# Optimization experiments

Hardware: AMD Instinct MI355X
Metric: run time of the kernel (lower is better)

## Reference

```python
import jax, jax.numpy as jnp
import numpy as np

T = 16000        # signal length
N1 = 120         # first-order filters (J=12, Q=10)
NPSI2 = 14       # second-order filterbank size (Q2=1)
NPAIR = 553      # second-order coefficients -> 120 + 553 = 673 channels
SUB1 = 8         # subsample U1 before order 2
T2 = T // SUB1   # 2000
STR1 = 1000      # lowpass stride at length T  -> 16 output samples
STR2 = T2 // (T // STR1)  # 125 -> 16 output samples
LOG_EPS = 1e-6
BN_EPS = 1e-5


def _gauss_hat(N, xi, sigma):
    om = np.arange(N) / N
    return np.exp(-((om - xi) ** 2) / (2.0 * sigma ** 2)).astype(np.float32)


def _filterbank():
    Q = 10.0
    xi1 = 0.45 * 2.0 ** (-np.arange(N1) / Q)
    sig1 = np.maximum(xi1 * 0.1, 2.0 / T)
    psi1 = np.stack([_gauss_hat(T, x, s) for x, s in zip(xi1, sig1)])
    phi1 = _gauss_hat(T, 0.0, 0.4 / STR1)
    xi2 = 0.45 * 2.0 ** (-np.arange(NPSI2, dtype=np.float64))
    sig2 = np.maximum(xi2 * 0.2, 2.0 / T2)
    psi2 = np.stack([_gauss_hat(T2, x, s) for x, s in zip(xi2, sig2)])
    phi2 = _gauss_hat(T2, 0.0, 0.4 / STR2)
    pairs = [(i, j) for i in range(N1) for j in range(NPSI2) if xi2[j] < xi1[i] / 2.0]
    pairs = pairs[:NPAIR]
    assert len(pairs) == NPAIR
    pi1 = np.array([p[0] for p in pairs], np.int32)
    pi2 = np.array([p[1] for p in pairs], np.int32)
    return psi1, phi1, psi2, phi2, pi1, pi2


def setup_inputs():
    key = jax.random.key(0)
    ks = jax.random.split(key, 8)
    psi1, phi1, psi2, phi2, pi1, pi2 = _filterbank()
    B = 32
    inp = {
        "x": jax.random.normal(ks[0], (B, 1, T), jnp.float32),
        "psi1_hat": jnp.asarray(psi1),
        "phi1_hat": jnp.asarray(phi1),
        "psi2_hat": jnp.asarray(psi2),
        "phi2_hat": jnp.asarray(phi2),
        "gamma": jnp.ones((673,), jnp.float32),
        "beta": jnp.zeros((673,), jnp.float32),
        "W1": jax.random.normal(ks[1], (300, 673), jnp.float32) * 0.04,
        "b1": jnp.zeros((300,), jnp.float32),
        "W2": jax.random.normal(ks[2], (90, 300), jnp.float32) * 0.06,
        "b2": jnp.zeros((90,), jnp.float32),
        "W3": jax.random.normal(ks[3], (35, 90), jnp.float32) * 0.1,
        "b3": jnp.zeros((35,), jnp.float32),
        "pair_i1": jnp.asarray(pi1),
        "pair_i2": jnp.asarray(pi2),
    }
    return inp


def reference(x, psi1_hat, phi1_hat, psi2_hat, phi2_hat, gamma, beta,
              W1, b1, W2, b2, W3, b3, pair_i1, pair_i2):
    xs = x.squeeze(1)                                       # [B, T]
    Xf = jnp.fft.fft(xs)                                    # [B, T] c64
    # --- order 1: wavelet conv (freq-domain), modulus ---
    U1 = jnp.abs(jnp.fft.ifft(Xf[:, None, :] * psi1_hat[None]))        # [B, N1, T]
    # S1 = lowpass(U1) subsampled to 16 samples
    S1 = jnp.real(jnp.fft.ifft(jnp.fft.fft(U1) * phi1_hat))[..., ::STR1]  # [B, N1, 16]
    # --- order 2 on subsampled U1 ---
    U1sf = jnp.fft.fft(U1[..., ::SUB1])                     # [B, N1, T2]
    U2 = jnp.abs(jnp.fft.ifft(U1sf[:, pair_i1, :] * psi2_hat[pair_i2]))  # [B, NPAIR, T2]
    S2 = jnp.real(jnp.fft.ifft(jnp.fft.fft(U2) * phi2_hat))[..., ::STR2]  # [B, NPAIR, 16]
    S = jnp.concatenate([S1, S2], axis=1)                   # [B, 673, 16]
    # log-abs + temporal mean pooling
    f = jnp.mean(jnp.log(jnp.abs(S) + LOG_EPS), axis=-1)    # [B, 673]
    # BatchNorm1d (training mode: batch statistics)
    mu = jnp.mean(f, axis=0)
    var = jnp.var(f, axis=0)
    f = (f - mu) / jnp.sqrt(var + BN_EPS) * gamma + beta
    # MLP head
    h = jax.nn.relu(f @ W1.T + b1)
    h = jax.nn.relu(h @ W2.T + b2)
    return jax.nn.log_softmax(h @ W3.T + b3, axis=-1)
```

## Files before the change

kernel.cpp:

```cpp
#include <hip/hip_runtime.h>
#include <math.h>

typedef float2 cf;

__device__ __forceinline__ cf cadd(cf a, cf b){ return make_float2(a.x+b.x, a.y+b.y); }
__device__ __forceinline__ cf csub(cf a, cf b){ return make_float2(a.x-b.x, a.y-b.y); }
__device__ __forceinline__ cf cmul(cf a, cf b){ return make_float2(a.x*b.x - a.y*b.y, a.x*b.y + a.y*b.x); }

__device__ __forceinline__ int SW(int i){ return i ^ ((i>>4)&15); }
#define AT(x) s[SW(x)]
#define WFENCE asm volatile("" ::: "memory")

template<bool WAVE> __device__ __forceinline__ void SYf(){
  if constexpr (WAVE) { WFENCE; } else __syncthreads();
}

__device__ __forceinline__ int devB(int i){
  int jm = i/10 + 2;
  double kc = 900.0*exp2((double)(-jm));
  double sg = fmax(180.0*exp2((double)(-jm)), 2.0);
  return min(2000, (int)ceil(kc + 6.5*sg) + 1);
}

template<int N, int L, bool INV>
__device__ __forceinline__ void stage_r2(cf* __restrict__ s, const cf* __restrict__ tw, int tid, int nt){
  constexpr int Ls = L/2, nbf = N/2, tws = 16000/L;
  for (int q = tid; q < nbf; q += nt){
    int blk = q / Ls, j = q - blk*Ls;
    int base = blk*L + j;
    cf w1 = tw[tws*j]; if (INV) w1.y = -w1.y;
    if (!INV){
      cf a = AT(base), b = AT(base+Ls);
      AT(base) = cadd(a,b);
      AT(base+Ls) = cmul(csub(a,b), w1);
    } else {
      cf a = AT(base), b = cmul(AT(base+Ls), w1);
      AT(base) = cadd(a,b);
      AT(base+Ls) = csub(a,b);
    }
  }
}

template<int N, int L, bool INV>
__device__ __forceinline__ void stage_r4(cf* __restrict__ s, const cf* __restrict__ tw, int tid, int nt){
  constexpr int Ls = L/4, nbf = N/4, tws = 16000/L;
  for (int q = tid; q < nbf; q += nt){
    int blk = q / Ls, j = q - blk*Ls;
    int base = blk*L + j;
    cf w1 = tw[tws*j]; if (INV) w1.y = -w1.y;
    cf w2 = cmul(w1,w1), w3 = cmul(w2,w1);
    if (!INV){
      cf y0=AT(base), y1=AT(base+Ls), y2=AT(base+2*Ls), y3=AT(base+3*Ls);
      cf t0=cadd(y0,y2), t1=csub(y0,y2), t2=cadd(y1,y3), t3=csub(y1,y3);
      AT(base)      = cadd(t0,t2);
      AT(base+Ls)   = cmul(make_float2(t1.x + t3.y, t1.y - t3.x), w1);
      AT(base+2*Ls) = cmul(csub(t0,t2), w2);
      AT(base+3*Ls) = cmul(make_float2(t1.x - t3.y, t1.y + t3.x), w3);
    } else {
      cf z0=AT(base);
      cf z1=cmul(AT(base+Ls),   w1);
      cf z2=cmul(AT(base+2*Ls), w2);
      cf z3=cmul(AT(base+3*Ls), w3);
      cf t0=cadd(z0,z2), t1=csub(z0,z2), t2=cadd(z1,z3), t3=csub(z1,z3);
      AT(base)      = cadd(t0,t2);
      AT(base+Ls)   = make_float2(t1.x - t3.y, t1.y + t3.x);
      AT(base+2*Ls) = csub(t0,t2);
      AT(base+3*Ls) = make_float2(t1.x + t3.y, t1.y - t3.x);
    }
  }
}

template<int N, int L, bool INV>
__device__ __forceinline__ void stage_r5(cf* __restrict__ s, const cf* __restrict__ tw, int tid, int nt){
  constexpr int Ls = L/5, nbf = N/5, tws = 16000/L;
  const float C1 = 0.30901699437494742f, S1c = 0.95105651629515357f;
  const float C2 = -0.80901699437494745f, S2c = 0.58778525229247314f;
  for (int q = tid; q < nbf; q += nt){
    int blk = q / Ls, j = q - blk*Ls;
    int base = blk*L + j;
    cf w1 = tw[tws*j]; if (INV) w1.y = -w1.y;
    cf w2 = cmul(w1,w1), w3 = cmul(w2,w1), w4 = cmul(w2,w2);
    if (!INV){
      cf y0=AT(base), y1=AT(base+Ls), y2=AT(base+2*Ls), y3=AT(base+3*Ls), y4=AT(base+4*Ls);
      cf t1=cadd(y1,y4), t2=csub(y1,y4), t3=cadd(y2,y3), t4=csub(y2,y3);
      cf z0 = cadd(y0, cadd(t1,t3));
      cf m1 = make_float2(y0.x + C1*t1.x + C2*t3.x, y0.y + C1*t1.y + C2*t3.y);
      cf m2 = make_float2(y0.x + C2*t1.x + C1*t3.x, y0.y + C2*t1.y + C1*t3.y);
      cf wa = make_float2(S1c*t2.x + S2c*t4.x, S1c*t2.y + S2c*t4.y);
      cf wb = make_float2(S2c*t2.x - S1c*t4.x, S2c*t2.y - S1c*t4.y);
      cf o1 = make_float2(m1.x + wa.y, m1.y - wa.x);
      cf o4 = make_float2(m1.x - wa.y, m1.y + wa.x);
      cf o2 = make_float2(m2.x + wb.y, m2.y - wb.x);
      cf o3 = make_float2(m2.x - wb.y, m2.y + wb.x);
      AT(base) = z0;
      AT(base+Ls)   = cmul(o1,w1);
      AT(base+2*Ls) = cmul(o2,w2);
      AT(base+3*Ls) = cmul(o3,w3);
      AT(base+4*Ls) = cmul(o4,w4);
    } else {
      cf z0=AT(base);
      cf z1=cmul(AT(base+Ls),   w1);
      cf z2=cmul(AT(base+2*Ls), w2);
      cf z3=cmul(AT(base+3*Ls), w3);
      cf z4=cmul(AT(base+4*Ls), w4);
      cf t1=cadd(z1,z4), t2=csub(z1,z4), t3=cadd(z2,z3), t4=csub(z2,z3);
      cf y0 = cadd(z0, cadd(t1,t3));
      cf m1 = make_float2(z0.x + C1*t1.x + C2*t3.x, z0.y + C1*t1.y + C2*t3.y);
      cf m2 = make_float2(z0.x + C2*t1.x + C1*t3.x, z0.y + C2*t1.y + C1*t3.y);
      cf wa = make_float2(S1c*t2.x + S2c*t4.x, S1c*t2.y + S2c*t4.y);
      cf wb = make_float2(S2c*t2.x - S1c*t4.x, S2c*t2.y - S1c*t4.y);
      AT(base)      = y0;
      AT(base+Ls)   = make_float2(m1.x - wa.y, m1.y + wa.x);
      AT(base+2*Ls) = make_float2(m2.x - wb.y, m2.y + wb.x);
      AT(base+3*Ls) = make_float2(m2.x + wb.y, m2.y - wb.x);
      AT(base+4*Ls) = make_float2(m1.x + wa.y, m1.y - wa.x);
    }
  }
}

template<int N, int L, bool INV>
__device__ __forceinline__ void stage_r8(cf* __restrict__ s, const cf* __restrict__ tw, int tid, int nt){
  constexpr int Ls = L/8, nbf = N/8, tws = 16000/L;
  const float RC = 0.70710678118654752f;
  for (int q = tid; q < nbf; q += nt){
    int blk = q / Ls, j = q - blk*Ls;
    int base = blk*L + j;
    cf w1 = tw[tws*j]; if (INV) w1.y = -w1.y;
    cf w2 = cmul(w1,w1), w3 = cmul(w2,w1), w4 = cmul(w2,w2);
    cf w5 = cmul(w4,w1), w6 = cmul(w3,w3), w7 = cmul(w4,w3);
    if (!INV){
      cf y0=AT(base), y1=AT(base+Ls), y2=AT(base+2*Ls), y3=AT(base+3*Ls);
      cf y4=AT(base+4*Ls), y5=AT(base+5*Ls), y6=AT(base+6*Ls), y7=AT(base+7*Ls);
      cf b0=cadd(y0,y4), b1=csub(y0,y4);
      cf b2=cadd(y2,y6), b3=csub(y2,y6);
      cf b4=cadd(y1,y5), b5=csub(y1,y5);
      cf b6=cadd(y3,y7), b7=csub(y3,y7);
      cf r3 = make_float2(b3.y, -b3.x);
      cf r7 = make_float2(b7.y, -b7.x);
      cf c0=cadd(b0,b2), c1=csub(b0,b2);
      cf c2=cadd(b1,r3), c3=csub(b1,r3);
      cf c4=cadd(b4,b6), c5=csub(b4,b6);
      cf c6=cadd(b5,r7), c7=csub(b5,r7);
      cf r5 = make_float2(c5.y, -c5.x);
      cf wc6 = make_float2(RC*(c6.x + c6.y), RC*(c6.y - c6.x));
      cf wc7 = make_float2(RC*(c7.y - c7.x), RC*(-c7.y - c7.x));
      AT(base)      = cadd(c0,c4);
      AT(base+Ls)   = cmul(cadd(c2,wc6), w1);
      AT(base+2*Ls) = cmul(cadd(c1,r5),  w2);
      AT(base+3*Ls) = cmul(cadd(c3,wc7), w3);
      AT(base+4*Ls) = cmul(csub(c0,c4),  w4);
      AT(base+5*Ls) = cmul(csub(c2,wc6), w5);
      AT(base+6*Ls) = cmul(csub(c1,r5),  w6);
      AT(base+7*Ls) = cmul(csub(c3,wc7), w7);
    } else {
      cf z0=AT(base);
      cf z1=cmul(AT(base+Ls),   w1);
      cf z2=cmul(AT(base+2*Ls), w2);
      cf z3=cmul(AT(base+3*Ls), w3);
      cf z4=cmul(AT(base+4*Ls), w4);
      cf z5=cmul(AT(base+5*Ls), w5);
      cf z6=cmul(AT(base+6*Ls), w6);
      cf z7=cmul(AT(base+7*Ls), w7);
      cf b0=cadd(z0,z4), b1=csub(z0,z4);
      cf b2=cadd(z2,z6), b3=csub(z2,z6);
      cf b4=cadd(z1,z5), b5=csub(z1,z5);
      cf b6=cadd(z3,z7), b7=csub(z3,z7);
      cf r3 = make_float2(-b3.y, b3.x);
      cf r7 = make_float2(-b7.y, b7.x);
      cf c0=cadd(b0,b2), c1=csub(b0,b2);
      cf c2=cadd(b1,r3), c3=csub(b1,r3);
      cf c4=cadd(b4,b6), c5=csub(b4,b6);
      cf c6=cadd(b5,r7), c7=csub(b5,r7);
      cf r5 = make_float2(-c5.y, c5.x);
      cf wc6 = make_float2(RC*(c6.x - c6.y), RC*(c6.x + c6.y));
      cf wc7 = make_float2(RC*(-c7.x - c7.y), RC*(c7.x - c7.y));
      AT(base)      = cadd(c0,c4);
      AT(base+Ls)   = cadd(c2,wc6);
      AT(base+2*Ls) = cadd(c1,r5);
      AT(base+3*Ls) = cadd(c3,wc7);
      AT(base+4*Ls) = csub(c0,c4);
      AT(base+5*Ls) = csub(c2,wc6);
      AT(base+6*Ls) = csub(c1,r5);
      AT(base+7*Ls) = csub(c3,wc7);
    }
  }
}

template<bool INV>
__device__ void fft16000(cf* s, const cf* tw, int tid, int nt){
  if (!INV){
    stage_r5<16000,16000,false>(s,tw,tid,nt); __syncthreads();
    stage_r5<16000, 3200,false>(s,tw,tid,nt); __syncthreads();
    stage_r5<16000,  640,false>(s,tw,tid,nt); __syncthreads();
    stage_r8<16000,  128,false>(s,tw,tid,nt); __syncthreads();
    stage_r4<16000,   16,false>(s,tw,tid,nt); __syncthreads();
    stage_r4<16000,    4,false>(s,tw,tid,nt); __syncthreads();
  } else {
    stage_r4<16000,    4,true >(s,tw,tid,nt); __syncthreads();
    stage_r4<16000,   16,true >(s,tw,tid,nt); __syncthreads();
    stage_r8<16000,  128,true >(s,tw,tid,nt); __syncthreads();
    stage_r5<16000,  640,true >(s,tw,tid,nt); __syncthreads();
    stage_r5<16000, 3200,true >(s,tw,tid,nt); __syncthreads();
    stage_r5<16000,16000,true >(s,tw,tid,nt); __syncthreads();
  }
}

template<bool INV>
__device__ void fft2000(cf* s, const cf* tw, int tid, int nt){
  if (!INV){
    stage_r5<2000,2000,false>(s,tw,tid,nt); __syncthreads();
    stage_r5<2000, 400,false>(s,tw,tid,nt); __syncthreads();
    stage_r5<2000,  80,false>(s,tw,tid,nt); __syncthreads();
    stage_r4<2000,  16,false>(s,tw,tid,nt); __syncthreads();
    stage_r4<2000,   4,false>(s,tw,tid,nt); __syncthreads();
  } else {
    stage_r4<2000,   4,true >(s,tw,tid,nt); __syncthreads();
    stage_r4<2000,  16,true >(s,tw,tid,nt); __syncthreads();
    stage_r5<2000,  80,true >(s,tw,tid,nt); __syncthreads();
    stage_r5<2000, 400,true >(s,tw,tid,nt); __syncthreads();
    stage_r5<2000,2000,true >(s,tw,tid,nt); __syncthreads();
  }
}

__device__ void fft8000i(cf* s, const cf* tw, int tid, int nt){
  stage_r8<8000,   8,true>(s,tw,tid,nt); __syncthreads();
  stage_r8<8000,  64,true>(s,tw,tid,nt); __syncthreads();
  stage_r5<8000, 320,true>(s,tw,tid,nt); __syncthreads();
  stage_r5<8000,1600,true>(s,tw,tid,nt); __syncthreads();
  stage_r5<8000,8000,true>(s,tw,tid,nt); __syncthreads();
}
__device__ void fft4000i(cf* s, const cf* tw, int tid, int nt){
  stage_r4<4000,   4,true>(s,tw,tid,nt); __syncthreads();
  stage_r8<4000,  32,true>(s,tw,tid,nt); __syncthreads();
  stage_r5<4000, 160,true>(s,tw,tid,nt); __syncthreads();
  stage_r5<4000, 800,true>(s,tw,tid,nt); __syncthreads();
  stage_r5<4000,4000,true>(s,tw,tid,nt); __syncthreads();
}
__device__ void fft4000f(cf* s, const cf* tw, int tid, int nt){
  stage_r5<4000,4000,false>(s,tw,tid,nt); __syncthreads();
  stage_r5<4000, 800,false>(s,tw,tid,nt); __syncthreads();
  stage_r5<4000, 160,false>(s,tw,tid,nt); __syncthreads();
  stage_r8<4000,  32,false>(s,tw,tid,nt); __syncthreads();
  stage_r4<4000,   4,false>(s,tw,tid,nt); __syncthreads();
}
__device__ void fft500i(cf* s, const cf* tw, int tid, int nt){
  stage_r4<500,  4,true>(s,tw,tid,nt); __syncthreads();
  stage_r5<500, 20,true>(s,tw,tid,nt); __syncthreads();
  stage_r5<500,100,true>(s,tw,tid,nt); __syncthreads();
  stage_r5<500,500,true>(s,tw,tid,nt); __syncthreads();
}
__device__ void fft1000i(cf* s, const cf* tw, int tid, int nt){
  stage_r8<1000,   8,true>(s,tw,tid,nt); __syncthreads();
  stage_r5<1000,  40,true>(s,tw,tid,nt); __syncthreads();
  stage_r5<1000, 200,true>(s,tw,tid,nt); __syncthreads();
  stage_r5<1000,1000,true>(s,tw,tid,nt); __syncthreads();
}
__device__ __forceinline__ void fft250w(cf* s, const cf* tw, int lane){
  stage_r2<250,  2,true>(s,tw,lane,64); WFENCE;
  stage_r5<250, 10,true>(s,tw,lane,64); WFENCE;
  stage_r5<250, 50,true>(s,tw,lane,64); WFENCE;
  stage_r5<250,250,true>(s,tw,lane,64); WFENCE;
}
__device__ __forceinline__ void fft125w(cf* s, const cf* tw, int lane){
  stage_r5<125,  5,true>(s,tw,lane,64); WFENCE;
  stage_r5<125, 25,true>(s,tw,lane,64); WFENCE;
  stage_r5<125,125,true>(s,tw,lane,64); WFENCE;
}

template<int M, bool INV, bool WAVE>
__device__ __forceinline__ void fftg(cf* s, const cf* tw, int tid, int nt){
  if constexpr (M==2000){
    if constexpr (INV){
      stage_r4<2000,4,true>(s,tw,tid,nt); SYf<WAVE>();
      stage_r4<2000,16,true>(s,tw,tid,nt); SYf<WAVE>();
      stage_r5<2000,80,true>(s,tw,tid,nt); SYf<WAVE>();
      stage_r5<2000,400,true>(s,tw,tid,nt); SYf<WAVE>();
      stage_r5<2000,2000,true>(s,tw,tid,nt); SYf<WAVE>();
    } else {
      stage_r5<2000,2000,false>(s,tw,tid,nt); SYf<WAVE>();
      stage_r5<2000,400,false>(s,tw,tid,nt); SYf<WAVE>();
      stage_r5<2000,80,false>(s,tw,tid,nt); SYf<WAVE>();
      stage_r4<2000,16,false>(s,tw,tid,nt); SYf<WAVE>();
      stage_r4<2000,4,false>(s,tw,tid,nt); SYf<WAVE>();
    }
  } else if constexpr (M==1600){
    if constexpr (INV){
      stage_r8<1600,8,true>(s,tw,tid,nt); SYf<WAVE>();
      stage_r8<1600,64,true>(s,tw,tid,nt); SYf<WAVE>();
      stage_r5<1600,320,true>(s,tw,tid,nt); SYf<WAVE>();
      stage_r5<1600,1600,true>(s,tw,tid,nt); SYf<WAVE>();
    } else {
      stage_r5<1600,1600,false>(s,tw,tid,nt); SYf<WAVE>();
      stage_r5<1600,320,false>(s,tw,tid,nt); SYf<WAVE>();
      stage_r8<1600,64,false>(s,tw,tid,nt); SYf<WAVE>();
      stage_r8<1600,8,false>(s,tw,tid,nt); SYf<WAVE>();
    }
  } else if constexpr (M==640){
    if constexpr (INV){
      stage_r4<640,4,true>(s,tw,tid,nt); SYf<WAVE>();
      stage_r4<640,16,true>(s,tw,tid,nt); SYf<WAVE>();
      stage_r8<640,128,true>(s,tw,tid,nt); SYf<WAVE>();
      stage_r5<640,640,true>(s,tw,tid,nt); SYf<WAVE>();
    } else {
      stage_r5<640,640,false>(s,tw,tid,nt); SYf<WAVE>();
      stage_r8<640,128,false>(s,tw,tid,nt); SYf<WAVE>();
      stage_r4<640,16,false>(s,tw,tid,nt); SYf<WAVE>();
      stage_r4<640,4,false>(s,tw,tid,nt); SYf<WAVE>();
    }
  } else if constexpr (M==320){
    if constexpr (INV){
      stage_r8<320,8,true>(s,tw,tid,nt); SYf<WAVE>();
      stage_r8<320,64,true>(s,tw,tid,nt); SYf<WAVE>();
      stage_r5<320,320,true>(s,tw,tid,nt); SYf<WAVE>();
    } else {
      stage_r5<320,320,false>(s,tw,tid,nt); SYf<WAVE>();
      stage_r8<320,64,false>(s,tw,tid,nt); SYf<WAVE>();
      stage_r8<320,8,false>(s,tw,tid,nt); SYf<WAVE>();
    }
  } else if constexpr (M==200){
    if constexpr (INV){
      stage_r8<200,8,true>(s,tw,tid,nt); SYf<WAVE>();
      stage_r5<200,40,true>(s,tw,tid,nt); SYf<WAVE>();
      stage_r5<200,200,true>(s,tw,tid,nt); SYf<WAVE>();
    } else {
      stage_r5<200,200,false>(s,tw,tid,nt); SYf<WAVE>();
      stage_r5<200,40,false>(s,tw,tid,nt); SYf<WAVE>();
      stage_r8<200,8,false>(s,tw,tid,nt); SYf<WAVE>();
    }
  } else {
    if constexpr (INV){
      stage_r4<160,4,true>(s,tw,tid,nt); SYf<WAVE>();
      stage_r8<160,32,true>(s,tw,tid,nt); SYf<WAVE>();
      stage_r5<160,160,true>(s,tw,tid,nt); SYf<WAVE>();
    } else {
      stage_r5<160,160,false>(s,tw,tid,nt); SYf<WAVE>();
      stage_r8<160,32,false>(s,tw,tid,nt); SYf<WAVE>();
      stage_r4<160,4,false>(s,tw,tid,nt); SYf<WAVE>();
    }
  }
}

__device__ __forceinline__ int pos16000(int k){
  int k0=k%5; k/=5; int k1=k%5; k/=5; int k2=k%5; k/=5;
  int k3=k&7; k>>=3; int k4=k&3; k>>=2;
  return k0*3200 + k1*640 + k2*128 + k3*16 + k4*4 + k;
}
__device__ __forceinline__ int pos8000(int k){
  int k0=k%5; k/=5; int k1=k%5; k/=5; int k2=k%5; k/=5;
  int k3=k&7, k4=k>>3;
  return k0*1600 + k1*320 + k2*64 + k3*8 + k4;
}
__device__ __forceinline__ int pos4000(int k){
  int k0=k%5; k/=5; int k1=k%5; k/=5; int k2=k%5; k/=5;
  int k3=k&7, k4=k>>3;
  return k0*800 + k1*160 + k2*32 + k3*4 + k4;
}
__device__ __forceinline__ int pos2000(int k){
  int k0=k%5; k/=5; int k1=k%5; k/=5; int k2=k%5; k/=5;
  int k3=k&3, k4=k>>2;
  return k0*400 + k1*80 + k2*16 + k3*4 + k4;
}
__device__ __forceinline__ int pos1600(int k){
  int k0=k%5; k/=5; int k1=k%5; k/=5;
  int k2=k&7; k>>=3;
  return k0*320 + k1*64 + k2*8 + k;
}
__device__ __forceinline__ int pos1000(int k){
  int k0=k%5; k/=5; int k1=k%5; k/=5; int k2=k%5; k/=5;
  return k0*200 + k1*40 + k2*8 + k;
}
__device__ __forceinline__ int pos640(int k){
  int k0=k%5; k/=5;
  int k1=k&7; k>>=3; int k2=k&3; k>>=2;
  return k0*128 + k1*16 + k2*4 + k;
}
__device__ __forceinline__ int pos500(int k){
  int k0=k%5; k/=5; int k1=k%5; k/=5; int k2=k%5; k/=5;
  return k0*100 + k1*20 + k2*4 + k;
}
__device__ __forceinline__ int pos320(int k){
  int k0=k%5; k/=5;
  int k1=k&7; k>>=3;
  return k0*64 + k1*8 + k;
}
__device__ __forceinline__ int pos250(int k){
  int k0=k%5; k/=5; int k1=k%5; k/=5; int k2=k%5; k/=5;
  return k0*50 + k1*10 + k2*2 + k;
}
__device__ __forceinline__ int pos125(int k){
  int k0=k%5; k/=5; int k1=k%5; k/=5;
  return k0*25 + k1*5 + k;
}
__device__ __forceinline__ int pos200(int k){
  int k0=k%5; k/=5; int k1=k%5; k/=5;
  return k0*40 + k1*8 + k;
}
__device__ __forceinline__ int pos160(int k){
  int k0=k%5; k/=5;
  int k1=k&7; k>>=3;
  return k0*32 + k1*4 + k;
}

template<int M> __device__ __forceinline__ int posM(int k){
  if constexpr (M==16000) return pos16000(k);
  else if constexpr (M==8000) return pos8000(k);
  else if constexpr (M==4000) return pos4000(k);
  else return pos2000(k);
}
template<int M> __device__ __forceinline__ int posN(int k){
  if constexpr (M==2000) return pos2000(k);
  else if constexpr (M==1600) return pos1600(k);
  else if constexpr (M==640) return pos640(k);
  else if constexpr (M==320) return pos320(k);
  else if constexpr (M==200) return pos200(k);
  else return pos160(k);
}
template<int M> __device__ __forceinline__ void fftM_inv(cf* s, const cf* tw, int tid, int nt){
  if constexpr (M==16000) fft16000<true>(s,tw,tid,nt);
  else if constexpr (M==8000) fft8000i(s,tw,tid,nt);
  else if constexpr (M==4000) fft4000i(s,tw,tid,nt);
  else fft2000<true>(s,tw,tid,nt);
}


__global__ void k_tw(cf* __restrict__ tw){
  int j = blockIdx.x*blockDim.x + threadIdx.x;
  if (j < 16000){
    double a = -6.283185307179586476925286766559 * (double)j / 16000.0;
    tw[j] = make_float2((float)cos(a), (float)sin(a));
  }
}

__global__ void k_btab(const float* __restrict__ phi1, const float* __restrict__ phi2,
                       float* __restrict__ h1g, float* __restrict__ h2g){
  int i = blockIdx.x*blockDim.x + threadIdx.x;
  const double TWO_PI = 6.283185307179586476925286766559;
  if (i < 5201){
    int d = i - 2600;
    double a = 0.0;
    for (int k = 0; k < 64; ++k) a += (double)phi1[k]*cos(TWO_PI*(double)(k*d)/16000.0);
    h1g[i] = (float)(a/16000.0 - (double)phi1[0]/32000.0);
  } else if (i == 5201){
    h1g[5201] = phi1[0]*(1.f/32000.f);
  } else if (i < 5202 + 661){
    int j = i - 5202; int d = j - 330;
    double a = 0.0;
    for (int k = 0; k < 64; ++k) a += (double)phi2[k]*cos(TWO_PI*(double)(k*d)/2000.0);
    h2g[j] = (float)(a/2000.0 - (double)phi2[0]/4000.0);
  } else if (i == 5202 + 661){
    h2g[661] = phi2[0]*(1.f/4000.f);
  }
}

__global__ __launch_bounds__(1024) void k_classify(const int* __restrict__ pi2,
                                                   int* __restrict__ list5, int* __restrict__ list4){
  __shared__ int w5[16], w4[16];
  int p = threadIdx.x;
  for (int t = p; t < 493; t += 1024) list5[t] = 0;
  for (int t = p; t < 60;  t += 1024) list4[t] = 0;
  bool valid = p < 553;
  int j2 = valid ? pi2[p] : 99;
  bool f5 = valid && (j2 >= 5);
  bool f4 = valid && (j2 < 5);
  unsigned long long m5 = __ballot(f5);
  unsigned long long m4 = __ballot(f4);
  int lane = p & 63, wid = p >> 6;
  if (lane == 0){ w5[wid] = __popcll(m5); w4[wid] = __popcll(m4); }
  __syncthreads();
  if (valid){
    int b5 = 0, b4 = 0;
    for (int w = 0; w < wid; ++w){ b5 += w5[w]; b4 += w4[w]; }
    unsigned long long lm = (1ull << lane) - 1ull;
    if (f5) list5[b5 + __popcll(m5 & lm)] = p;
    if (f4) list4[b4 + __popcll(m4 & lm)] = p;
  }
}

__global__ __launch_bounds__(512) void k_fftx4(const float* __restrict__ x, cf* __restrict__ Xf,
                                               const cf* __restrict__ tw){
  extern __shared__ cf s[];
  int blk = blockIdx.x;
  int b = blk >> 2, r = blk & 3;
  int tid = threadIdx.x;
  const float* xb = x + (size_t)b*16000;
  for (int j = tid; j < 4000; j += 512){
    float x0 = xb[j], x1 = xb[j+4000], x2 = xb[j+8000], x3 = xb[j+12000];
    cf f;
    if (r == 0)      f = make_float2(x0 + x1 + x2 + x3, 0.f);
    else if (r == 1) f = make_float2(x0 - x2, x3 - x1);
    else if (r == 2) f = make_float2(x0 - x1 + x2 - x3, 0.f);
    else             f = make_float2(x0 - x2, x1 - x3);
    cf y = (r == 0) ? f : cmul(f, tw[j*r]);
    AT(j) = y;
  }
  __syncthreads();
  fft4000f(s, tw, tid, 512);
  cf* out = Xf + (size_t)b*16000 + r;
  for (int m = tid; m < 4000; m += 512) out[4*m] = AT(pos4000(m));
}

template<int M, int ST, int NF, int I0, int NT>
__global__ __launch_bounds__(NT) void kf(const cf* __restrict__ Xf, const float* __restrict__ psi1,
                                         const float* __restrict__ h1g, const cf* __restrict__ tw,
                                         cf* __restrict__ U1sf, float* __restrict__ S1){
  extern __shared__ cf s[];
  constexpr int NW = NT/64;
  int b = blockIdx.x / NF;
  int i = I0 + (blockIdx.x - b*NF);
  int tid = threadIdx.x, wid = tid>>6, lane = tid&63;
  double x1 = 0.45 * exp2((double)(-i) / 10.0);
  double kc = 16000.0 * x1;
  double sg = fmax(1600.0 * x1, 2.0);
  int k0 = max(0, (int)floor(kc - 6.5*sg));
  int k1 = min(16000, (int)ceil(kc + 6.5*sg) + 1);
  int W = k1 - k0;
  for (int n = tid; n < M; n += NT) s[n] = make_float2(0.f, 0.f);
  __syncthreads();
  const cf* X = Xf + (size_t)b*16000 + k0;
  const float* P = psi1 + (size_t)i*16000 + k0;
  for (int j = tid; j < W; j += NT){
    cf v = X[j]; float pf = P[j];
    int pp = posM<M>(j);
    AT(pp) = make_float2(v.x*pf, v.y*pf);
  }
  __syncthreads();
  fftM_inv<M>(s, tw, tid, NT);
  constexpr int R = (M + NT - 1)/NT;
  float mreg[R]; float tsum = 0.f;
  const float inv = 1.f/16000.f;
  #pragma unroll
  for (int r = 0; r < R; ++r){
    int n = tid + r*NT;
    if (n < M){ cf v = AT(n); mreg[r] = sqrtf(v.x*v.x + v.y*v.y)*inv; tsum += mreg[r]; }
    else mreg[r] = 0.f;
  }
  float* fl = (float*)s;
  float* part = (float*)(s + M);
  __syncthreads();
  #pragma unroll
  for (int r = 0; r < R; ++r){ int n = tid + r*NT; if (n < M) fl[n] = mreg[r]; }
  #pragma unroll
  for (int o = 32; o > 0; o >>= 1) tsum += __shfl_xor(tsum, o);
  if (lane == 0) part[wid] = tsum;
  __syncthreads();
  if (tid == 0){ float tt = 0.f; for (int w = 0; w < NW; ++w) tt += part[w]; part[NW] = tt; }
  __syncthreads();
  float stot = part[NW];
  float c1 = h1g[5201];
  for (int t = wid; t < 16; t += NW){
    int mlo = (1000*t - 2600)/ST;
    int mhi = (1000*t + 2600)/ST;
    float acc = 0.f;
    for (int m = mlo + lane; m <= mhi; m += 64){
      int mm = m; if (mm < 0) mm += M; else if (mm >= M) mm -= M;
      acc = fmaf(fl[mm], h1g[1000*t - m*ST + 2600], acc);
    }
    #pragma unroll
    for (int o = 32; o > 0; o >>= 1) acc += __shfl_xor(acc, o);
    if (lane == 0) S1[((size_t)b*120 + i)*16 + t] = (float)ST*(acc + c1*stot);
  }
  constexpr int K = 8/ST;
  float d0 = fl[tid*K];
  float d1 = 0.f;
  { int m2 = tid + 1024; if (m2 < 2000) d1 = fl[m2*K]; }
  __syncthreads();
  AT(tid) = make_float2(d0, 0.f);
  { int m2 = tid + 1024; if (m2 < 2000) AT(m2) = make_float2(d1, 0.f); }
  __syncthreads();
  fft2000<false>(s, tw, tid, NT);
  int B = devB(i);
  cf* out = U1sf + ((size_t)b*120 + i)*2000;
  for (int k = tid; k < B; k += NT) out[k] = AT(pos2000(k));
}

template<int M, int NF, int I0>
__global__ __launch_bounds__(256) void k_n2(const cf* __restrict__ Xf, const float* __restrict__ psi1,
                                            const float* __restrict__ phi1, const cf* __restrict__ tw,
                                            cf* __restrict__ U1sf, float* __restrict__ S1){
  extern __shared__ cf s[];
  int b = blockIdx.x / NF;
  int i = I0 + (blockIdx.x - b*NF);
  int tid = threadIdx.x, wid = tid>>6, lane = tid&63;
  double x1 = 0.45 * exp2((double)(-i)/10.0);
  double kc = 16000.0*x1, sg = fmax(1600.0*x1, 2.0);
  int k0 = max(0,(int)floor(kc-6.5*sg));
  int k1 = min(16000,(int)ceil(kc+6.5*sg)+1);
  int W = k1-k0;
  for (int n = tid; n < M; n += 256) s[n] = make_float2(0.f,0.f);
  __syncthreads();
  const cf* X = Xf + (size_t)b*16000 + k0;
  const float* P = psi1 + (size_t)i*16000 + k0;
  for (int j = tid; j < W; j += 256){
    cf v = X[j]; float pf = P[j];
    AT(posN<M>(j)) = make_float2(v.x*pf, v.y*pf);
  }
  __syncthreads();
  fftg<M,true,false>(s,tw,tid,256);
  for (int n = tid; n < M; n += 256){
    cf v = AT(n);
    AT(n) = make_float2(sqrtf(v.x*v.x+v.y*v.y)*(1.f/16000.f), 0.f);
  }
  __syncthreads();
  fftg<M,false,false>(s,tw,tid,256);
  {
    int k = lane;
    cf g = AT(posN<M>(k));
    float ph = phi1[k];
    float gx = g.x*ph, gy = g.y*ph;
    float* S1o = S1 + ((size_t)b*120+i)*16;
    for (int r = 0; r < 4; ++r){
      int t = wid + 4*r;
      cf e = tw[1000*((k*t)&15)];
      float val = gx*e.x + gy*e.y;
      #pragma unroll
      for (int o = 32; o > 0; o >>= 1) val += __shfl_xor(val, o);
      if (lane == 0) S1o[t] = val*(1.f/(float)M);
    }
  }
  int B = devB(i);
  const float sc = 2000.f/(float)M;
  cf* out = U1sf + ((size_t)b*120+i)*2000;
  for (int k = tid; k < B; k += 256){
    cf v = AT(posN<M>(k));
    out[k] = make_float2(v.x*sc, v.y*sc);
  }
}

template<int M, int SPAD, int NF, int I0, int WPB>
__global__ __launch_bounds__(WPB*64) void k_nw2(const cf* __restrict__ Xf, const float* __restrict__ psi1,
                                                const float* __restrict__ phi1, const cf* __restrict__ tw,
                                                cf* __restrict__ U1sf, float* __restrict__ S1){
  extern __shared__ cf sh[];
  int wid = threadIdx.x >> 6, lane = threadIdx.x & 63;
  int q = blockIdx.x*WPB + wid;
  int filt = q >> 5, b = q & 31;
  int i = I0 + filt;
  cf* s = sh + wid*SPAD;
  double x1 = 0.45 * exp2((double)(-i)/10.0);
  double kc = 16000.0*x1, sg = fmax(1600.0*x1, 2.0);
  int k0 = max(0,(int)floor(kc-6.5*sg));
  int k1 = min(16000,(int)ceil(kc+6.5*sg)+1);
  int W = k1-k0;
  for (int n = lane; n < SPAD; n += 64) s[n] = make_float2(0.f,0.f);
  WFENCE;
  const cf* X = Xf + (size_t)b*16000 + k0;
  const float* P = psi1 + (size_t)i*16000 + k0;
  for (int j = lane; j < W; j += 64){
    cf v = X[j]; float pf = P[j];
    AT(posN<M>(j)) = make_float2(v.x*pf, v.y*pf);
  }
  WFENCE;
  fftg<M,true,true>(s,tw,lane,64);
  for (int n = lane; n < M; n += 64){
    cf v = AT(n);
    AT(n) = make_float2(sqrtf(v.x*v.x+v.y*v.y)*(1.f/16000.f), 0.f);
  }
  WFENCE;
  fftg<M,false,true>(s,tw,lane,64);
  {
    int k = lane;
    cf g = AT(posN<M>(k));
    float ph = phi1[k];
    float gx = g.x*ph, gy = g.y*ph;
    float* S1o = S1 + ((size_t)b*120+i)*16;
    for (int t = 0; t < 16; ++t){
      cf e = tw[1000*((k*t)&15)];
      float val = gx*e.x + gy*e.y;
      #pragma unroll
      for (int o = 32; o > 0; o >>= 1) val += __shfl_xor(val, o);
      if (lane == 0) S1o[t] = val*(1.f/(float)M);
    }
  }
  int B = devB(i);
  const float sc = 2000.f/(float)M;
  cf* out = U1sf + ((size_t)b*120+i)*2000;
  for (int k = lane; k < B; k += 64){
    cf v = AT(posN<M>(k));
    out[k] = make_float2(v.x*sc, v.y*sc);
  }
}

__global__ __launch_bounds__(256) void k_sec5(const cf* __restrict__ U1sf, const float* __restrict__ psi2,
                                              const float* __restrict__ h2g, const cf* __restrict__ tw,
                                              const int* __restrict__ pi1, const int* __restrict__ pi2,
                                              const int* __restrict__ list5, float* __restrict__ S2){
  __shared__ cf sall[4*256];
  __shared__ float flall[4*256];
  int wid = threadIdx.x >> 6, lane = threadIdx.x & 63;
  int q = blockIdx.x*4 + wid;
  int p = list5[q >> 5];
  int b = q & 31;
  int i1 = pi1[p], j2 = pi2[p];
  cf* s = sall + wid*256;
  float* fl2 = flall + wid*256;
  int M2  = (j2 >= 6) ? 125 : 250;
  int s2l = (j2 >= 6) ? 4 : 3;
  double xc = exp2((double)(-j2));
  double kc = 900.0*xc, sg = fmax(180.0*xc, 2.0);
  int k0 = max(0, (int)floor(kc - 6.5*sg));
  int k1 = min(2000, (int)ceil(kc + 6.5*sg) + 1);
  int W = k1 - k0;
  for (int n = lane; n < 256; n += 64) s[n] = make_float2(0.f, 0.f);
  WFENCE;
  const cf* U = U1sf + (size_t)(b*120 + i1)*2000 + k0;
  const float* F = psi2 + j2*2000 + k0;
  for (int j = lane; j < W; j += 64){
    cf v = U[j]; float f = F[j];
    int pp = (M2 == 125) ? pos125(j) : pos250(j);
    AT(pp) = make_float2(v.x*f, v.y*f);
  }
  WFENCE;
  if (M2 == 125) fft125w(s, tw, lane); else fft250w(s, tw, lane);
  float tsum = 0.f;
  #pragma unroll
  for (int r = 0; r < 4; ++r){
    int n = lane + r*64;
    if (n < M2){
      cf v = AT(n);
      float mg = sqrtf(v.x*v.x + v.y*v.y)*(1.f/2000.f);
      fl2[n] = mg; tsum += mg;
    }
  }
  WFENCE;
  #pragma unroll
  for (int o = 32; o > 0; o >>= 1) tsum += __shfl_xor(tsum, o);
  float stot = tsum;
  float c2 = h2g[661];
  float scale = (float)(1 << s2l);
  float* S2o = S2 + (size_t)(b*553 + p)*16;
  int g16 = lane >> 4, li = lane & 15;
  for (int r = 0; r < 4; ++r){
    int t = g16*4 + r;
    int x0 = 125*t - 330, x1b = 125*t + 330;
    int mlo = (x0 + ((1<<s2l)-1)) >> s2l;
    int mhi = x1b >> s2l;
    float acc = 0.f;
    for (int m = mlo + li; m <= mhi; m += 16){
      int mm = m; if (mm < 0) mm += M2; else if (mm >= M2) mm -= M2;
      acc = fmaf(fl2[mm], h2g[125*t - (m << s2l) + 330], acc);
    }
    #pragma unroll
    for (int o = 8; o > 0; o >>= 1) acc += __shfl_xor(acc, o);
    if (li == 0) S2o[t] = scale*(acc + c2*stot);
  }
}

__global__ __launch_bounds__(128) void k_secbig(const cf* __restrict__ U1sf, const float* __restrict__ psi2,
                                                const float* __restrict__ h2g, const cf* __restrict__ tw,
                                                const int* __restrict__ pi1, const int* __restrict__ pi2,
                                                const int* __restrict__ list4, float* __restrict__ S2){
  extern __shared__ cf s[];
  float* fl2 = (float*)(s + 2000);
  float* part = fl2 + 2000;
  int p = list4[blockIdx.x >> 5];
  int b = blockIdx.x & 31;
  int tid = threadIdx.x, wid = tid>>6, lane = tid&63;
  int i1 = pi1[p], j2 = pi2[p];
  int M2, s2l;
  if (j2 == 4){ M2 = 500;  s2l = 2; }
  else if (j2 == 3){ M2 = 1000; s2l = 1; }
  else { M2 = 2000; s2l = 0; }
  int ST2 = 1 << s2l;
  double xc = exp2((double)(-j2));
  double kc = 900.0*xc, sg = fmax(180.0*xc, 2.0);
  int k0 = max(0, (int)floor(kc - 6.5*sg));
  int k1 = min(2000, (int)ceil(kc + 6.5*sg) + 1);
  int W = k1 - k0;
  int M2r = (M2 + 15) & ~15;
  for (int n = tid; n < M2r; n += 128) s[n] = make_float2(0.f, 0.f);
  __syncthreads();
  const cf* U = U1sf + (size_t)(b*120 + i1)*2000 + k0;
  const float* F = psi2 + j2*2000 + k0;
  for (int j = tid; j < W; j += 128){
    cf v = U[j]; float f = F[j];
    int pp;
    if (M2 == 500) pp = pos500(j);
    else if (M2 == 1000) pp = pos1000(j);
    else pp = pos2000(j);
    AT(pp) = make_float2(v.x*f, v.y*f);
  }
  __syncthreads();
  if (M2 == 500) fft500i(s, tw, tid, 128);
  else if (M2 == 1000) fft1000i(s, tw, tid, 128);
  else fft2000<true>(s, tw, tid, 128);
  float tsum = 0.f;
  for (int n = tid; n < M2; n += 128){
    cf v = AT(n);
    float mg = sqrtf(v.x*v.x + v.y*v.y)*(1.f/2000.f);
    fl2[n] = mg; tsum += mg;
  }
  #pragma unroll
  for (int o = 32; o > 0; o >>= 1) tsum += __shfl_xor(tsum, o);
  if (lane == 0) part[wid] = tsum;
  __syncthreads();
  float stot = part[0] + part[1];
  float c2 = h2g[661];
  float* S2o = S2 + (size_t)(b*553 + p)*16;
  for (int r = 0; r < 8; ++r){
    int t = wid + (r<<1);
    int mlo = (125*t - 330 + ST2 - 1) >> s2l;
    int mhi = (125*t + 330) >> s2l;
    float acc = 0.f;
    for (int m = mlo + lane; m <= mhi; m += 64){
      int mm = m; if (mm < 0) mm += M2; else if (mm >= M2) mm -= M2;
      acc = fmaf(fl2[mm], h2g[125*t - m*ST2 + 330], acc);
    }
    #pragma unroll
    for (int o = 32; o > 0; o >>= 1) acc += __shfl_xor(acc, o);
    if (lane == 0) S2o[t] = (float)ST2*(acc + c2*stot);
  }
}

__global__ __launch_bounds__(64) void k_fbn(const float* __restrict__ S1, const float* __restrict__ S2,
                                            const float* __restrict__ g, const float* __restrict__ be,
                                            float* __restrict__ fn){
  int j = blockIdx.x;
  int b = threadIdx.x;
  float f = 0.f;
  if (b < 32){
    const float* src = (j < 120) ? (S1 + (b*120 + j)*16) : (S2 + (b*553 + (j-120))*16);
    float acc = 0.f;
    #pragma unroll
    for (int t = 0; t < 16; ++t) acc += logf(fabsf(src[t]) + 1e-6f);
    f = acc * (1.f/16.f);
  }
  float mu = f;
  #pragma unroll
  for (int o = 16; o > 0; o >>= 1) mu += __shfl_xor(mu, o);
  mu *= (1.f/32.f);
  float d = f - mu;
  float v = d*d;
  #pragma unroll
  for (int o = 16; o > 0; o >>= 1) v += __shfl_xor(v, o);
  v *= (1.f/32.f);
  float is = g[j] / sqrtf(v + 1e-5f);
  if (b < 32) fn[b*673 + j] = d*is + be[j];
}

__global__ __launch_bounds__(512) void k_mlp1(const float* __restrict__ fn,
                                              const float* __restrict__ W1, const float* __restrict__ b1,
                                              float* __restrict__ h1o){
  int task = blockIdx.x*8 + (threadIdx.x >> 6);
  int lane = threadIdx.x & 63;
  if (task >= 32*300) return;
  int b = task / 300, r = task - b*300;
  const float* f = fn + b*673;
  const float* w = W1 + r*673;
  float acc = 0.f;
  for (int k = lane; k < 673; k += 64) acc = fmaf(f[k], w[k], acc);
  #pragma unroll
  for (int o = 32; o > 0; o >>= 1) acc += __shfl_down(acc, o);
  if (lane == 0) h1o[b*300 + r] = fmaxf(acc + b1[r], 0.f);
}

__global__ __launch_bounds__(512) void k_mlp2(const float* __restrict__ h1,
                                              const float* __restrict__ W2, const float* __restrict__ b2,
                                              float* __restrict__ h2o){
  int task = blockIdx.x*8 + (threadIdx.x >> 6);
  int lane = threadIdx.x & 63;
  if (task >= 32*90) return;
  int b = task / 90, r = task - b*90;
  const float* h = h1 + b*300;
  const float* w = W2 + r*300;
  float acc = 0.f;
  for (int k = lane; k < 300; k += 64) acc = fmaf(h[k], w[k], acc);
  #pragma unroll
  for (int o = 32; o > 0; o >>= 1) acc += __shfl_down(acc, o);
  if (lane == 0) h2o[b*90 + r] = fmaxf(acc + b2[r], 0.f);
}

__global__ __launch_bounds__(256) void k_mlp3(const float* __restrict__ h2,
                                              const float* __restrict__ W3, const float* __restrict__ b3,
                                              float* __restrict__ out){
  __shared__ float lg[35];
  int b = blockIdx.x;
  int tid = threadIdx.x, wid = tid >> 6, lane = tid & 63;
  for (int r = wid; r < 35; r += 4){
    float acc = 0.f;
    for (int k = lane; k < 90; k += 64) acc = fmaf(h2[b*90 + k], W3[r*90 + k], acc);
    #pragma unroll
    for (int o = 32; o > 0; o >>= 1) acc += __shfl_down(acc, o);
    if (lane == 0) lg[r] = acc + b3[r];
  }
  __syncthreads();
  if (tid < 64){
    float v = (tid < 35) ? lg[tid] : -1e30f;
    float mx = v;
    #pragma unroll
    for (int o = 32; o > 0; o >>= 1) mx = fmaxf(mx, __shfl_xor(mx, o));
    float e = (tid < 35) ? expf(v - mx) : 0.f;
    float se = e;
    #pragma unroll
    for (int o = 32; o > 0; o >>= 1) se += __shfl_xor(se, o);
    if (tid < 35) out[b*35 + tid] = v - mx - logf(se);
  }
}


extern "C" void kernel_launch(void* const* d_in, const int* in_sizes, int n_in,
                              void* d_out, int out_size, void* d_ws, size_t ws_size,
                              hipStream_t stream){
  const float* x     = (const float*)d_in[0];
  const float* psi1  = (const float*)d_in[1];
  const float* phi1  = (const float*)d_in[2];
  const float* psi2  = (const float*)d_in[3];
  const float* phi2  = (const float*)d_in[4];
  const float* gamma = (const float*)d_in[5];
  const float* beta  = (const float*)d_in[6];
  const float* W1    = (const float*)d_in[7];
  const float* b1    = (const float*)d_in[8];
  const float* W2    = (const float*)d_in[9];
  const float* b2    = (const float*)d_in[10];
  const float* W3    = (const float*)d_in[11];
  const float* b3    = (const float*)d_in[12];
  const int*   pi1   = (const int*)d_in[13];
  const int*   pi2   = (const int*)d_in[14];

  char* ws = (char*)d_ws;
  constexpr size_t o_tw = 0;
  constexpr size_t o_Xf = o_tw + (size_t)16000*sizeof(cf);
  constexpr size_t o_U  = o_Xf + (size_t)32*16000*sizeof(cf);
  constexpr size_t o_S1 = o_U  + (size_t)3840*2000*sizeof(cf);
  constexpr size_t o_S2 = o_S1 + (size_t)3840*16*sizeof(float);
  constexpr size_t o_l5 = o_S2 + (size_t)17696*16*sizeof(float);
  constexpr size_t o_l4 = o_l5 + (size_t)512*sizeof(int);
  constexpr size_t o_fn = o_l4 + (size_t)64*sizeof(int);
  constexpr size_t o_h1 = o_fn + (size_t)32*673*sizeof(float);
  constexpr size_t o_h2 = o_h1 + (size_t)5202*sizeof(float);
  constexpr size_t o_m1 = o_h2 + (size_t)662*sizeof(float);
  constexpr size_t o_m2 = o_m1 + (size_t)32*300*sizeof(float);

  cf*    tw    = (cf*)(ws + o_tw);
  cf*    Xf    = (cf*)(ws + o_Xf);
  cf*    U1sf  = (cf*)(ws + o_U);
  float* S1b   = (float*)(ws + o_S1);
  float* S2b   = (float*)(ws + o_S2);
  int*   list5 = (int*)(ws + o_l5);
  int*   list4 = (int*)(ws + o_l4);
  float* fnbuf = (float*)(ws + o_fn);
  float* h1g   = (float*)(ws + o_h1);
  float* h2g   = (float*)(ws + o_h2);
  float* m1buf = (float*)(ws + o_m1);
  float* m2buf = (float*)(ws + o_m2);

  hipFuncSetAttribute((const void*)kf<16000,1,13, 0,1024>, hipFuncAttributeMaxDynamicSharedMemorySize, 131072);
  hipFuncSetAttribute((const void*)kf< 8000,2,10,13,1024>, hipFuncAttributeMaxDynamicSharedMemorySize, 131072);

  k_tw<<<63, 256, 0, stream>>>(tw);
  k_btab<<<23, 256, 0, stream>>>(phi1, phi2, h1g, h2g);
  k_classify<<<1, 1024, 0, stream>>>(pi2, list5, list4);
  k_fftx4<<<128, 512, 4000*8, stream>>>(x, Xf, tw);
  kf<16000,1,13, 0,1024><<<32*13, 1024, 16000*8 + 17*4, stream>>>(Xf, psi1, h1g, tw, U1sf, S1b);
  kf< 8000,2,10,13,1024><<<32*10, 1024,  8000*8 + 17*4, stream>>>(Xf, psi1, h1g, tw, U1sf, S1b);
  kf< 4000,4,10,23,1024><<<32*10, 1024,  4000*8 + 17*4, stream>>>(Xf, psi1, h1g, tw, U1sf, S1b);
  k_n2<2000,10,33><<<32*10, 256, 2000*8, stream>>>(Xf, psi1, phi1, tw, U1sf, S1b);
  k_n2<1600,10,43><<<32*10, 256, 1600*8, stream>>>(Xf, psi1, phi1, tw, U1sf, S1b);
  k_nw2<640,640,10,53,4><<< 80, 256, 4*640*8, stream>>>(Xf, psi1, phi1, tw, U1sf, S1b);
  k_nw2<320,320,10,63,8><<< 40, 512, 8*320*8, stream>>>(Xf, psi1, phi1, tw, U1sf, S1b);
  k_nw2<200,208,10,73,8><<< 40, 512, 8*208*8, stream>>>(Xf, psi1, phi1, tw, U1sf, S1b);
  k_nw2<160,160,37,83,8><<<148, 512, 8*160*8, stream>>>(Xf, psi1, phi1, tw, U1sf, S1b);
  k_sec5<<<(493*32)/4, 256, 0, stream>>>(U1sf, psi2, h2g, tw, pi1, pi2, list5, S2b);
  k_secbig<<<60*32, 128, 2000*8 + 2000*4 + 4*4, stream>>>(U1sf, psi2, h2g, tw, pi1, pi2, list4, S2b);
  k_fbn<<<673, 64, 0, stream>>>(S1b, S2b, gamma, beta, fnbuf);
  k_mlp1<<<1200, 512, 0, stream>>>(fnbuf, W1, b1, m1buf);
  k_mlp2<<<360, 512, 0, stream>>>(m1buf, W2, b2, m2buf);
  k_mlp3<<<32, 256, 0, stream>>>(m2buf, W3, b3, (float*)d_out);
}
```

Baseline: 335.5 us.

## Split 16000-point first-order filters into four 4000-point inverse FFTs plus reduction kernel

Replaces the single 1024-thread, 128KB-LDS kernel that ran full 16000-point inverse FFTs for the 13 widest first-order filters with two kernels. The first uses a radix-4 decimation split: four blocks per (batch, filter) each run a 4000-point inverse FFT in 32KB of LDS and write the modulus plus a partial sum. The second gathers the interleaved modulus, computes the lowpass S1 outputs and the subsampled 2000-point forward FFT. The aim is more, smaller blocks with better occupancy, at the cost of an extra global round trip for a 416x16000 float buffer and an extra launch.

```diff
diff --git a/kernel.cpp b/kernel.cpp
--- a/kernel.cpp
+++ b/kernel.cpp
@@ -6,6 +6,7 @@
 __device__ __forceinline__ cf cadd(cf a, cf b){ return make_float2(a.x+b.x, a.y+b.y); }
 __device__ __forceinline__ cf csub(cf a, cf b){ return make_float2(a.x-b.x, a.y-b.y); }
 __device__ __forceinline__ cf cmul(cf a, cf b){ return make_float2(a.x*b.x - a.y*b.y, a.x*b.y + a.y*b.x); }
+__device__ __forceinline__ cf cmulc(cf a, cf b){ return make_float2(a.x*b.x + a.y*b.y, a.y*b.x - a.x*b.y); }
 
 __device__ __forceinline__ int SW(int i){ return i ^ ((i>>4)&15); }
 #define AT(x) s[SW(x)]
@@ -187,25 +188,6 @@
 }
 
 template<bool INV>
-__device__ void fft16000(cf* s, const cf* tw, int tid, int nt){
-  if (!INV){
-    stage_r5<16000,16000,false>(s,tw,tid,nt); __syncthreads();
-    stage_r5<16000, 3200,false>(s,tw,tid,nt); __syncthreads();
-    stage_r5<16000,  640,false>(s,tw,tid,nt); __syncthreads();
-    stage_r8<16000,  128,false>(s,tw,tid,nt); __syncthreads();
-    stage_r4<16000,   16,false>(s,tw,tid,nt); __syncthreads();
-    stage_r4<16000,    4,false>(s,tw,tid,nt); __syncthreads();
-  } else {
-    stage_r4<16000,    4,true >(s,tw,tid,nt); __syncthreads();
-    stage_r4<16000,   16,true >(s,tw,tid,nt); __syncthreads();
-    stage_r8<16000,  128,true >(s,tw,tid,nt); __syncthreads();
-    stage_r5<16000,  640,true >(s,tw,tid,nt); __syncthreads();
-    stage_r5<16000, 3200,true >(s,tw,tid,nt); __syncthreads();
-    stage_r5<16000,16000,true >(s,tw,tid,nt); __syncthreads();
-  }
-}
-
-template<bool INV>
 __device__ void fft2000(cf* s, const cf* tw, int tid, int nt){
   if (!INV){
     stage_r5<2000,2000,false>(s,tw,tid,nt); __syncthreads();
@@ -340,11 +322,6 @@
   }
 }
 
-__device__ __forceinline__ int pos16000(int k){
-  int k0=k%5; k/=5; int k1=k%5; k/=5; int k2=k%5; k/=5;
-  int k3=k&7; k>>=3; int k4=k&3; k>>=2;
-  return k0*3200 + k1*640 + k2*128 + k3*16 + k4*4 + k;
-}
 __device__ __forceinline__ int pos8000(int k){
   int k0=k%5; k/=5; int k1=k%5; k/=5; int k2=k%5; k/=5;
   int k3=k&7, k4=k>>3;
@@ -402,8 +379,7 @@
 }
 
 template<int M> __device__ __forceinline__ int posM(int k){
-  if constexpr (M==16000) return pos16000(k);
-  else if constexpr (M==8000) return pos8000(k);
+  if constexpr (M==8000) return pos8000(k);
   else if constexpr (M==4000) return pos4000(k);
   else return pos2000(k);
 }
@@ -416,8 +392,7 @@
   else return pos160(k);
 }
 template<int M> __device__ __forceinline__ void fftM_inv(cf* s, const cf* tw, int tid, int nt){
-  if constexpr (M==16000) fft16000<true>(s,tw,tid,nt);
-  else if constexpr (M==8000) fft8000i(s,tw,tid,nt);
+  if constexpr (M==8000) fft8000i(s,tw,tid,nt);
   else if constexpr (M==4000) fft4000i(s,tw,tid,nt);
   else fft2000<true>(s,tw,tid,nt);
 }
@@ -497,6 +472,107 @@
   fft4000f(s, tw, tid, 512);
   cf* out = Xf + (size_t)b*16000 + r;
   for (int m = tid; m < 4000; m += 512) out[4*m] = AT(pos4000(m));
+}
+
+__global__ __launch_bounds__(512) void k_u1a(const cf* __restrict__ Xf, const float* __restrict__ psi1,
+                                             const cf* __restrict__ tw,
+                                             float* __restrict__ flbuf, float* __restrict__ partials){
+  extern __shared__ cf s[];
+  __shared__ float part[8];
+  int bi = blockIdx.x >> 2, r = blockIdx.x & 3;
+  int b = bi / 13, i = bi - b*13;
+  int tid = threadIdx.x, wid = tid>>6, lane = tid&63;
+  double x1 = 0.45 * exp2((double)(-i) / 10.0);
+  double kc = 16000.0 * x1;
+  double sg = fmax(1600.0 * x1, 2.0);
+  int k0 = max(0, (int)floor(kc - 6.5*sg));
+  int k1 = min(16000, (int)ceil(kc + 6.5*sg) + 1);
+  const cf* X = Xf + (size_t)b*16000;
+  const float* P = psi1 + (size_t)i*16000;
+  for (int j = tid; j < 4000; j += 512){
+    cf xq[4];
+    #pragma unroll
+    for (int q = 0; q < 4; ++q){
+      int k = j + 4000*q;
+      if (k >= k0 && k < k1){ cf v = X[k]; float p = P[k]; xq[q] = make_float2(v.x*p, v.y*p); }
+      else xq[q] = make_float2(0.f, 0.f);
+    }
+    cf f;
+    if (r == 0)      f = cadd(cadd(xq[0],xq[1]), cadd(xq[2],xq[3]));
+    else if (r == 1) f = make_float2((xq[0].x - xq[2].x) - (xq[1].y - xq[3].y),
+                                     (xq[0].y - xq[2].y) + (xq[1].x - xq[3].x));
+    else if (r == 2) f = cadd(csub(xq[0],xq[1]), csub(xq[2],xq[3]));
+    else             f = make_float2((xq[0].x - xq[2].x) + (xq[1].y - xq[3].y),
+                                     (xq[0].y - xq[2].y) - (xq[1].x - xq[3].x));
+    cf y = (r == 0) ? f : cmulc(f, tw[j*r]);
+    AT(pos4000(j)) = y;
+  }
+  __syncthreads();
+  fft4000i(s, tw, tid, 512);
+  float* out = flbuf + ((size_t)bi*4 + r)*4000;
+  const float inv = 1.f/16000.f;
+  float tsum = 0.f;
+  for (int m = tid; m < 4000; m += 512){
+    cf v = AT(m);
+    float mg = sqrtf(v.x*v.x + v.y*v.y)*inv;
+    out[m] = mg; tsum += mg;
+  }
+  #pragma unroll
+  for (int o = 32; o > 0; o >>= 1) tsum += __shfl_xor(tsum, o);
+  if (lane == 0) part[wid] = tsum;
+  __syncthreads();
+  if (tid == 0){
+    float tt = 0.f;
+    for (int w = 0; w < 8; ++w) tt += part[w];
+    partials[bi*4 + r] = tt;
+  }
+}
+
+__global__ __launch_bounds__(512) void k_u1b(const float* __restrict__ flbuf, const float* __restrict__ partials,
+                                             const float* __restrict__ h1g, const cf* __restrict__ tw,
+                                             cf* __restrict__ U1sf, float* __restrict__ S1){
+  extern __shared__ cf s[];
+  float* fl = (float*)s;
+  int bi = blockIdx.x;
+  int b = bi / 13, i = bi - b*13;
+  int tid = threadIdx.x, wid = tid>>6, lane = tid&63;
+  const float* src = flbuf + (size_t)bi*16000;
+  for (int t = tid; t < 16000; t += 512){
+    int r = t / 4000, m = t - r*4000;
+    fl[4*m + r] = src[t];
+  }
+  __syncthreads();
+  float stot = partials[bi*4] + partials[bi*4+1] + partials[bi*4+2] + partials[bi*4+3];
+  float c1 = h1g[5201];
+  for (int t = wid; t < 16; t += 8){
+    int mlo = 1000*t - 2600;
+    int mhi = 1000*t + 2600;
+    float acc = 0.f;
+    for (int m = mlo + lane; m <= mhi; m += 64){
+      int mm = m; if (mm < 0) mm += 16000; else if (mm >= 16000) mm -= 16000;
+      acc = fmaf(fl[mm], h1g[1000*t - m + 2600], acc);
+    }
+    #pragma unroll
+    for (int o = 32; o > 0; o >>= 1) acc += __shfl_xor(acc, o);
+    if (lane == 0) S1[((size_t)b*120 + i)*16 + t] = acc + c1*stot;
+  }
+  float d[4];
+  #pragma unroll
+  for (int u = 0; u < 4; ++u){
+    int m2 = tid + u*512;
+    d[u] = (m2 < 2000) ? fl[8*m2] : 0.f;
+  }
+  __syncthreads();
+  #pragma unroll
+  for (int u = 0; u < 4; ++u){
+    int m2 = tid + u*512;
+    if (m2 < 2000) AT(m2) = make_float2(d[u], 0.f);
+  }
+  __syncthreads();
+  fft2000<false>(s, tw, tid, 512);
+  int B = devB(i);
+  cf* out = U1sf + ((size_t)b*120 + i)*2000;
+  for (int k = tid; k < B; k += 512) out[k] = AT(pos2000(k));
 }
 
 template<int M, int ST, int NF, int I0, int NT>
@@ -929,6 +1005,8 @@
   constexpr size_t o_h2 = o_h1 + (size_t)5202*sizeof(float);
   constexpr size_t o_m1 = o_h2 + (size_t)662*sizeof(float);
   constexpr size_t o_m2 = o_m1 + (size_t)32*300*sizeof(float);
+  constexpr size_t o_fl = o_m2 + (size_t)32*90*sizeof(float);
+  constexpr size_t o_pt = o_fl + (size_t)416*16000*sizeof(float);
 
   cf*    tw    = (cf*)(ws + o_tw);
   cf*    Xf    = (cf*)(ws + o_Xf);
@@ -942,15 +1020,17 @@
   float* h2g   = (float*)(ws + o_h2);
   float* m1buf = (float*)(ws + o_m1);
   float* m2buf = (float*)(ws + o_m2);
-
-  hipFuncSetAttribute((const void*)kf<16000,1,13, 0,1024>, hipFuncAttributeMaxDynamicSharedMemorySize, 131072);
+  float* flbuf = (float*)(ws + o_fl);
+  float* ptbuf = (float*)(ws + o_pt);
+
   hipFuncSetAttribute((const void*)kf< 8000,2,10,13,1024>, hipFuncAttributeMaxDynamicSharedMemorySize, 131072);
 
   k_tw<<<63, 256, 0, stream>>>(tw);
   k_btab<<<23, 256, 0, stream>>>(phi1, phi2, h1g, h2g);
   k_classify<<<1, 1024, 0, stream>>>(pi2, list5, list4);
   k_fftx4<<<128, 512, 4000*8, stream>>>(x, Xf, tw);
-  kf<16000,1,13, 0,1024><<<32*13, 1024, 16000*8 + 17*4, stream>>>(Xf, psi1, h1g, tw, U1sf, S1b);
+  k_u1a<<<416*4, 512, 4000*8, stream>>>(Xf, psi1, tw, flbuf, ptbuf);
+  k_u1b<<<416, 512, 16000*4, stream>>>(flbuf, ptbuf, h1g, tw, U1sf, S1b);
   kf< 8000,2,10,13,1024><<<32*10, 1024,  8000*8 + 17*4, stream>>>(Xf, psi1, h1g, tw, U1sf, S1b);
   kf< 4000,4,10,23,1024><<<32*10, 1024,  4000*8 + 17*4, stream>>>(Xf, psi1, h1g, tw, U1sf, S1b);
   k_n2<2000,10,33><<<32*10, 256, 2000*8, stream>>>(Xf, psi1, phi1, tw, U1sf, S1b);
```

New measurement: 368.1 us. 1.1x slower.
